# Kernel optimization log

Hardware: AMD Instinct MI355X
Metric: run time of the kernel (lower is better)

Reference implementation:

```python
import jax, jax.numpy as jnp
import numpy as np

H = 1024
NH = 16
HD = H // NH
EPS = 1e-5


def setup_inputs() -> dict:
    key = jax.random.key(0)
    ks = jax.random.split(key, 12)
    B, S = 4, 2048
    scale = 1.0 / np.sqrt(H)
    inp = {
        "x": jax.random.normal(ks[0], (B, S, H), jnp.float32),
        "mask": jnp.ones((B, S), jnp.int32),
        "Wq": jax.random.normal(ks[1], (H, H), jnp.float32) * scale,
        "bq": jnp.zeros((H,), jnp.float32),
        "Wk": jax.random.normal(ks[2], (H, H), jnp.float32) * scale,
        "bk": jnp.zeros((H,), jnp.float32),
        "Wv": jax.random.normal(ks[3], (H, H), jnp.float32) * scale,
        "bv": jnp.zeros((H,), jnp.float32),
        "Wo": jax.random.normal(ks[4], (H, H), jnp.float32) * scale,
        "bo": jnp.zeros((H,), jnp.float32),
        "gamma": jnp.ones((H,), jnp.float32),
        "beta": jnp.zeros((H,), jnp.float32),
    }
    return inp


def reference(x, mask, Wq, bq, Wk, bk, Wv, bv, Wo, bo, gamma, beta):
    B, S, _ = x.shape
    # QKV projections -> [B, NH, S, HD]
    def split_heads(t):
        return t.reshape(B, S, NH, HD).transpose(0, 2, 1, 3)
    q = split_heads(x @ Wq.T + bq)
    k = split_heads(x @ Wk.T + bk)
    v = split_heads(x @ Wv.T + bv)
    # scaled dot-product scores [B, NH, S, S]
    scores = jnp.einsum("bhqd,bhkd->bhqk", q, k) / np.sqrt(HD).astype(np.float32)
    m = (mask[:, None, None, :] == 0)  # [B,1,1,S]
    scores = jnp.where(m, -1e9, scores)
    attn = jax.nn.softmax(scores, axis=-1)
    # dropout is identity at eval time
    attended = jnp.einsum("bhqk,bhkd->bhqd", attn, v)
    attended = attended.transpose(0, 2, 1, 3).reshape(B, S, H)
    out = attended @ Wo.T + bo
    # residual + LayerNorm
    y = x + out
    mu = jnp.mean(y, axis=-1, keepdims=True)
    var = jnp.mean(jnp.square(y - mu), axis=-1, keepdims=True)
    return (y - mu) * jax.lax.rsqrt(var + EPS) * gamma + beta
```

## Files before the change

### kernel.cpp

```cpp
#include <hip/hip_runtime.h>
#include <stdint.h>

#define HDIM 1024
#define NHEAD 16
#define HD 64
#define NB 4
#define SEQ 2048
#define NROWS (NB*SEQ)
#define NBH (NB*NHEAD)

typedef __attribute__((ext_vector_type(8))) short short8;
typedef __attribute__((ext_vector_type(4))) float f32x4;

typedef __attribute__((address_space(1))) const void gk_t;
typedef __attribute__((address_space(3))) void lds_t;

static __device__ __forceinline__ unsigned short f2bf(float f) {
  union { float f; unsigned u; } v; v.f = f;
  unsigned r = v.u + 0x7fffu + ((v.u >> 16) & 1u);
  return (unsigned short)(r >> 16);
}

__global__ __launch_bounds__(256) void cvt_f32_bf16(const float* __restrict__ in,
                                                    unsigned short* __restrict__ out,
                                                    int n4) {
  int i = blockIdx.x * 256 + threadIdx.x;
  if (i >= n4) return;
  float4 v = reinterpret_cast<const float4*>(in)[i];
  ushort4 o;
  o.x = f2bf(v.x); o.y = f2bf(v.y); o.z = f2bf(v.z); o.w = f2bf(v.w);
  reinterpret_cast<ushort4*>(out)[i] = o;
}

__global__ __launch_bounds__(256) void cvt_weights(
    const float* __restrict__ Wq, const float* __restrict__ Wk,
    const float* __restrict__ Wv, const float* __restrict__ Wo,
    unsigned short* __restrict__ wqkv, unsigned short* __restrict__ wo) {
  int which = blockIdx.x >> 10;
  int i = (blockIdx.x & 1023) * 256 + threadIdx.x;
  const float* src = (which == 0) ? Wq : (which == 1) ? Wk : (which == 2) ? Wv : Wo;
  unsigned short* dst = (which < 3) ? (wqkv + (size_t)which * 1048576) : wo;
  float4 v = reinterpret_cast<const float4*>(src)[i];
  ushort4 o;
  o.x = f2bf(v.x); o.y = f2bf(v.y); o.z = f2bf(v.z); o.w = f2bf(v.w);
  reinterpret_cast<ushort4*>(dst)[i] = o;
}

__global__ __launch_bounds__(256) void mask_prep(const int* __restrict__ mask,
                                                 float* __restrict__ fb,
                                                 unsigned* __restrict__ flags) {
  if (blockIdx.x < 32) {
    int i = blockIdx.x * 256 + threadIdx.x;
    fb[i] = (mask[i] == 0) ? -1e9f : 0.0f;
  } else {
    int i = threadIdx.x;
    __shared__ unsigned char sh[128];
    if (i < 128) {
      int b = i >> 5, t = i & 31;
      const int* mrow = mask + b * SEQ + t * 64;
      int any = 0;
#pragma unroll 8
      for (int j = 0; j < 64; ++j) any |= (mrow[j] == 0);
      sh[i] = (unsigned char)any;
    }
    __syncthreads();
    if (i < NB) {
      unsigned f = 0;
      for (int t2 = 0; t2 < 32; ++t2) f |= (sh[i * 32 + t2] ? 1u : 0u) << t2;
      flags[i] = f;
    }
  }
}

static __device__ __forceinline__ void gemm_mainloop(
    const unsigned short* __restrict__ A, const unsigned short* __restrict__ B,
    int rowA0, int rowB0,
    unsigned short* As, unsigned short* Bs,
    f32x4 acc[4][4]) {
  const int tid  = threadIdx.x;
  const int lane = tid & 63;
  const int wave = tid >> 6;
  const int wm = wave >> 1, wn = wave & 1;
  const int srow = lane >> 3;
  const int scol = (lane & 7) << 3;

  for (int kt = 0; kt < 1024; kt += 64) {
    __syncthreads();
#pragma unroll
    for (int i = 0; i < 4; ++i) {
      int c = wave * 4 + i;
      const unsigned short* ga = A + (size_t)(rowA0 + c * 8 + srow) * 1024 + kt + scol;
      const unsigned short* gb = B + (size_t)(rowB0 + c * 8 + srow) * 1024 + kt + scol;
      __builtin_amdgcn_global_load_lds((gk_t*)ga, (lds_t*)(As + c * 512), 16, 0, 0);
      __builtin_amdgcn_global_load_lds((gk_t*)gb, (lds_t*)(Bs + c * 512), 16, 0, 0);
    }
    __syncthreads();
#pragma unroll
    for (int kk = 0; kk < 2; ++kk) {
      short8 af[4], bfr[4];
#pragma unroll
      for (int mi = 0; mi < 4; ++mi)
        af[mi] = *reinterpret_cast<const short8*>(
            As + (wm * 64 + mi * 16 + (lane & 15)) * 64 + kk * 32 + ((lane >> 4) << 3));
#pragma unroll
      for (int ni = 0; ni < 4; ++ni)
        bfr[ni] = *reinterpret_cast<const short8*>(
            Bs + (wn * 64 + ni * 16 + (lane & 15)) * 64 + kk * 32 + ((lane >> 4) << 3));
#pragma unroll
      for (int mi = 0; mi < 4; ++mi)
#pragma unroll
        for (int ni = 0; ni < 4; ++ni)
          acc[mi][ni] = __builtin_amdgcn_mfma_f32_16x16x32_bf16(af[mi], bfr[ni], acc[mi][ni], 0, 0, 0);
    }
  }
}

__global__ __launch_bounds__(256) void gemm_qkv(
    const unsigned short* __restrict__ xb, const unsigned short* __restrict__ wqkv,
    const float* __restrict__ bq, const float* __restrict__ bk, const float* __restrict__ bv,
    unsigned short* __restrict__ qout, unsigned short* __restrict__ kout,
    unsigned short* __restrict__ vtout) {
  __shared__ __align__(16) unsigned short As[128 * 64];
  __shared__ __align__(16) unsigned short Bs[128 * 64];
  f32x4 acc[4][4];
  const f32x4 zero = {0.f, 0.f, 0.f, 0.f};
#pragma unroll
  for (int i = 0; i < 4; ++i)
#pragma unroll
    for (int j = 0; j < 4; ++j) acc[i][j] = zero;

  int flat = blockIdx.y * 24 + blockIdx.x;
  int s = (flat & 7) * 192 + (flat >> 3);
  int by = s / 24, bx = s - by * 24;
  const int bm0 = by * 128;
  const int bn0 = bx * 128;
  gemm_mainloop(xb, wqkv, bm0, bn0, As, Bs, acc);

  const int lane = threadIdx.x & 63, wave = threadIdx.x >> 6;
  const int wm = wave >> 1, wn = wave & 1;
#pragma unroll
  for (int mi = 0; mi < 4; ++mi) {
    int m0 = bm0 + wm * 64 + mi * 16 + ((lane >> 4) << 2);
#pragma unroll
    for (int ni = 0; ni < 4; ++ni) {
      int n = bn0 + wn * 64 + ni * 16 + (lane & 15);
      int which = n >> 10;
      int nc = n & 1023;
      float bias = (which == 0 ? bq : which == 1 ? bk : bv)[nc];
      int h = nc >> 6, d = nc & 63;
#pragma unroll
      for (int r = 0; r < 4; ++r) {
        int m = m0 + r;
        int b = m >> 11, ss = m & 2047;
        float v = acc[mi][ni][r] + bias;
        if (which == 0) v *= 0.18033688011112042f;
        unsigned short val = f2bf(v);
        int bh = b * NHEAD + h;
        if (which == 2) {
          vtout[(((size_t)bh * HD + d) << 11) + ss] = val;
        } else {
          unsigned short* dst = (which == 0) ? qout : kout;
          dst[(((size_t)bh << 11) + ss) * HD + d] = val;
        }
      }
    }
  }
}

__global__ __launch_bounds__(256) void gemm_proj(
    const unsigned short* __restrict__ ab, const unsigned short* __restrict__ wob,
    const float* __restrict__ bo, const float* __restrict__ x, float* __restrict__ y) {
  __shared__ __align__(16) unsigned short As[128 * 64];
  __shared__ __align__(16) unsigned short Bs[128 * 64];
  f32x4 acc[4][4];
  const f32x4 zero = {0.f, 0.f, 0.f, 0.f};
#pragma unroll
  for (int i = 0; i < 4; ++i)
#pragma unroll
    for (int j = 0; j < 4; ++j) acc[i][j] = zero;

  int flat = blockIdx.y * 8 + blockIdx.x;
  int s = (flat & 7) * 64 + (flat >> 3);
  int by = s >> 3, bx = s & 7;
  const int bm0 = by * 128;
  const int bn0 = bx * 128;
  gemm_mainloop(ab, wob, bm0, bn0, As, Bs, acc);

  const int lane = threadIdx.x & 63, wave = threadIdx.x >> 6;
  const int wm = wave >> 1, wn = wave & 1;
#pragma unroll
  for (int mi = 0; mi < 4; ++mi) {
    int m0 = bm0 + wm * 64 + mi * 16 + ((lane >> 4) << 2);
#pragma unroll
    for (int ni = 0; ni < 4; ++ni) {
      int n = bn0 + wn * 64 + ni * 16 + (lane & 15);
      float bias = bo[n];
#pragma unroll
      for (int r = 0; r < 4; ++r) {
        size_t idx = (size_t)(m0 + r) * HDIM + n;
        y[idx] = acc[mi][ni][r] + bias + x[idx];
      }
    }
  }
}

__global__ __launch_bounds__(512) void flash_attn(
    const unsigned short* __restrict__ Q, const unsigned short* __restrict__ K,
    const unsigned short* __restrict__ VT, const float* __restrict__ fbias,
    const unsigned* __restrict__ mflagsPtr,
    unsigned short* __restrict__ O) {
  __shared__ __align__(16) char Ks[2][64 * 128];
  __shared__ __align__(16) char Vs[2][64 * 128];
  __shared__ __align__(16) char Ps[8 * 16 * 128];

  const int tid = threadIdx.x;
  const int lane = tid & 63, wave = tid >> 6;
  const int l15 = lane & 15, g = lane >> 4;
  const int bh = blockIdx.y;
  const int b = bh >> 4, h = bh & 15;
  const int q0 = blockIdx.x * 128;

  const unsigned short* qptr = Q + ((size_t)bh * SEQ + q0 + wave * 16 + l15) * HD + g * 8;
  short8 qf0 = *reinterpret_cast<const short8*>(qptr);
  short8 qf1 = *reinterpret_cast<const short8*>(qptr + 32);

  const f32x4 zero = {0.f, 0.f, 0.f, 0.f};
  f32x4 oacc[4];
#pragma unroll
  for (int i = 0; i < 4; ++i) oacc[i] = zero;
  f32x4 lacc = zero;
  const unsigned mflags = mflagsPtr[b];

  short8 ones;
#pragma unroll
  for (int i = 0; i < 8; ++i) ones[i] = (short)0x3F80;

  const int srow = tid >> 3;
  const int scol = (tid & 7) << 3;
  const int swzs = (srow & 7) << 4;
  const int stoff = srow * 128 + ((scol * 2) ^ swzs);
  char* kd0 = Ks[0] + stoff; char* kd1 = Ks[1] + stoff;
  char* vd0 = Vs[0] + stoff; char* vd1 = Vs[1] + stoff;
  const unsigned short* kg = K + ((size_t)bh * SEQ + srow) * HD + scol;
  const unsigned short* vg = VT + (((size_t)bh * HD + srow) << 11) + scol;

  const int cfrag = g << 4;
  const int swzr = (l15 & 7) << 4;
  const float* fbrow = fbias + b * SEQ;
  char* prow = Ps + wave * 2048 + l15 * 128;

  short8 kp = *reinterpret_cast<const short8*>(kg);
  short8 vp = *reinterpret_cast<const short8*>(vg);
  *reinterpret_cast<short8*>(kd0) = kp;
  *reinterpret_cast<short8*>(vd0) = vp;
  kp = *reinterpret_cast<const short8*>(kg + (size_t)64 * HD);
  vp = *reinterpret_cast<const short8*>(vg + 64);
  __syncthreads();

  auto step = [&](int jt, const char* Kr, const char* Vr, char* Kw, char* Vw) {
    f32x4 sf[4];
    __builtin_amdgcn_s_setprio(1);
#pragma unroll
    for (int ni = 0; ni < 4; ++ni) {
      const char* kr = Kr + (ni * 16 + l15) * 128;
      short8 a0 = *reinterpret_cast<const short8*>(kr + (cfrag ^ swzr));
      short8 a1 = *reinterpret_cast<const short8*>(kr + ((cfrag + 64) ^ swzr));
      f32x4 t = __builtin_amdgcn_mfma_f32_16x16x32_bf16(a0, qf0, zero, 0, 0, 0);
      sf[ni] = __builtin_amdgcn_mfma_f32_16x16x32_bf16(a1, qf1, t, 0, 0, 0);
    }
    __builtin_amdgcn_s_setprio(0);

    if (jt + 1 < SEQ / 64) {
      *reinterpret_cast<short8*>(Kw) = kp;
      *reinterpret_cast<short8*>(Vw) = vp;
    }

    if (__builtin_amdgcn_readfirstlane((mflags >> jt) & 1u)) {
#pragma unroll
      for (int ni = 0; ni < 4; ++ni) {
        f32x4 fbv = *reinterpret_cast<const f32x4*>(fbrow + jt * 64 + ni * 16 + 4 * g);
#pragma unroll
        for (int r = 0; r < 4; ++r) sf[ni][r] += fbv[r];
      }
    }

#pragma unroll
    for (int ni = 0; ni < 4; ++ni)
#pragma unroll
      for (int r = 0; r < 4; ++r)
        sf[ni][r] = __builtin_amdgcn_exp2f(sf[ni][r]);

#pragma unroll
    for (int ni = 0; ni < 4; ++ni) {
      unsigned lo_, hi_;
      asm("v_cvt_pk_bf16_f32 %0, %1, %2" : "=v"(lo_) : "v"(sf[ni][0]), "v"(sf[ni][1]));
      asm("v_cvt_pk_bf16_f32 %0, %1, %2" : "=v"(hi_) : "v"(sf[ni][2]), "v"(sf[ni][3]));
      *reinterpret_cast<uint2*>(prow + ((32 * ni + 8 * g) ^ swzr)) = make_uint2(lo_, hi_);
    }
    asm volatile("s_waitcnt lgkmcnt(0)" ::: "memory");
    __builtin_amdgcn_sched_barrier(0);
    short8 pb0 = *reinterpret_cast<const short8*>(prow + (cfrag ^ swzr));
    short8 pb1 = *reinterpret_cast<const short8*>(prow + ((cfrag + 64) ^ swzr));

    __builtin_amdgcn_s_setprio(1);
#pragma unroll
    for (int di = 0; di < 4; ++di) {
      const char* vr = Vr + (di * 16 + l15) * 128;
      short8 va0 = *reinterpret_cast<const short8*>(vr + (cfrag ^ swzr));
      short8 va1 = *reinterpret_cast<const short8*>(vr + ((cfrag + 64) ^ swzr));
      oacc[di] = __builtin_amdgcn_mfma_f32_16x16x32_bf16(va0, pb0, oacc[di], 0, 0, 0);
      oacc[di] = __builtin_amdgcn_mfma_f32_16x16x32_bf16(va1, pb1, oacc[di], 0, 0, 0);
    }
    lacc = __builtin_amdgcn_mfma_f32_16x16x32_bf16(ones, pb0, lacc, 0, 0, 0);
    lacc = __builtin_amdgcn_mfma_f32_16x16x32_bf16(ones, pb1, lacc, 0, 0, 0);
    __builtin_amdgcn_s_setprio(0);

    if (jt + 2 < SEQ / 64) {
      kp = *reinterpret_cast<const short8*>(kg + (size_t)(jt + 2) * 64 * HD);
      vp = *reinterpret_cast<const short8*>(vg + (jt + 2) * 64);
    }
  };

  for (int jt = 0; jt < SEQ / 64; jt += 2) {
    step(jt,     Ks[0], Vs[0], kd1, vd1);
    __syncthreads();
    step(jt + 1, Ks[1], Vs[1], kd0, vd0);
    __syncthreads();
  }

  {
    float inv = 1.0f / lacc[0];
    char* orow_lds = Ps + (wave * 16 + l15) * 128;
#pragma unroll
    for (int di = 0; di < 4; ++di) {
      float e0 = oacc[di][0] * inv, e1 = oacc[di][1] * inv;
      float e2 = oacc[di][2] * inv, e3 = oacc[di][3] * inv;
      unsigned lo_, hi_;
      asm("v_cvt_pk_bf16_f32 %0, %1, %2" : "=v"(lo_) : "v"(e0), "v"(e1));
      asm("v_cvt_pk_bf16_f32 %0, %1, %2" : "=v"(hi_) : "v"(e2), "v"(e3));
      char* dst = orow_lds + ((32 * di + 8 * g) ^ swzr);
      *reinterpret_cast<uint2*>(dst) = make_uint2(lo_, hi_);
    }
  }
  __syncthreads();
  {
    int q = tid >> 2;
    int c4 = tid & 3;
    int swz = (q & 7) << 4;
    const char* src = Ps + q * 128;
    short8 o0 = *reinterpret_cast<const short8*>(src + ((c4 * 32) ^ swz));
    short8 o1 = *reinterpret_cast<const short8*>(src + ((c4 * 32 + 16) ^ swz));
    unsigned short* orow = O + ((size_t)b * SEQ + q0 + q) * HDIM + h * 64 + c4 * 16;
    *reinterpret_cast<short8*>(orow) = o0;
    *reinterpret_cast<short8*>(orow + 8) = o1;
  }
}

__global__ __launch_bounds__(256) void layernorm(float* __restrict__ y,
                                                 const float* __restrict__ gamma,
                                                 const float* __restrict__ beta) {
  const int row = blockIdx.x;
  float* yr = y + (size_t)row * HDIM;
  const int tid = threadIdx.x;
  float4 v = reinterpret_cast<const float4*>(yr)[tid];
  float s = v.x + v.y + v.z + v.w;
  float s2 = v.x * v.x + v.y * v.y + v.z * v.z + v.w * v.w;
#pragma unroll
  for (int off = 1; off < 64; off <<= 1) {
    s += __shfl_xor(s, off);
    s2 += __shfl_xor(s2, off);
  }
  __shared__ float red[8];
  const int wave = tid >> 6, lane = tid & 63;
  if (lane == 0) { red[wave] = s; red[wave + 4] = s2; }
  __syncthreads();
  s = red[0] + red[1] + red[2] + red[3];
  s2 = red[4] + red[5] + red[6] + red[7];
  float mean = s * (1.f / HDIM);
  float var = s2 * (1.f / HDIM) - mean * mean;
  float rstd = rsqrtf(var + 1e-5f);
  float4 g = reinterpret_cast<const float4*>(gamma)[tid];
  float4 bt = reinterpret_cast<const float4*>(beta)[tid];
  float4 o;
  o.x = (v.x - mean) * rstd * g.x + bt.x;
  o.y = (v.y - mean) * rstd * g.y + bt.y;
  o.z = (v.z - mean) * rstd * g.z + bt.z;
  o.w = (v.w - mean) * rstd * g.w + bt.w;
  reinterpret_cast<float4*>(yr)[tid] = o;
}

extern "C" void kernel_launch(void* const* d_in, const int* in_sizes, int n_in,
                              void* d_out, int out_size, void* d_ws, size_t ws_size,
                              hipStream_t stream) {
  (void)in_sizes; (void)n_in; (void)out_size; (void)ws_size;
  const float* x     = (const float*)d_in[0];
  const int*   mask  = (const int*)d_in[1];
  const float* Wq    = (const float*)d_in[2];
  const float* bq    = (const float*)d_in[3];
  const float* Wk    = (const float*)d_in[4];
  const float* bk    = (const float*)d_in[5];
  const float* Wv    = (const float*)d_in[6];
  const float* bv    = (const float*)d_in[7];
  const float* Wo    = (const float*)d_in[8];
  const float* bo    = (const float*)d_in[9];
  const float* gamma = (const float*)d_in[10];
  const float* beta  = (const float*)d_in[11];
  float* out = (float*)d_out;

  char* ws = (char*)d_ws;
  unsigned short* xb   = (unsigned short*)(ws);
  unsigned short* wqkv = (unsigned short*)(ws + 16777216);
  unsigned short* wo   = (unsigned short*)(ws + 16777216 + 6291456);
  unsigned short* q    = (unsigned short*)(ws + 25165824);
  unsigned short* k    = (unsigned short*)(ws + 25165824 + 16777216);
  unsigned short* vt   = (unsigned short*)(ws + 25165824 + 2 * 16777216);
  unsigned short* attn = xb;
  float* fbias = (float*)(ws + 16777216);
  unsigned* mflags = (unsigned*)(ws + 16777216 + NB * SEQ * 4);

  cvt_f32_bf16<<<8192, 256, 0, stream>>>(x, xb, NROWS * HDIM / 4);
  cvt_weights<<<4096, 256, 0, stream>>>(Wq, Wk, Wv, Wo, wqkv, wo);

  gemm_qkv<<<dim3(24, 64), 256, 0, stream>>>(xb, wqkv, bq, bk, bv, q, k, vt);
  mask_prep<<<33, 256, 0, stream>>>(mask, fbias, mflags);
  flash_attn<<<dim3(16, 64), 512, 0, stream>>>(q, k, vt, fbias, mflags, attn);
  gemm_proj<<<dim3(8, 64), 256, 0, stream>>>(attn, wo, bo, x, out);
  layernorm<<<NROWS, 256, 0, stream>>>(out, gamma, beta);
}
```

Before: 247.2 us.

## Double-buffer GEMM mainloop with swizzled LDS and 256-row tiles

Replaces the GEMM mainloop with a 256x128 tile version run by 512 threads (8 waves). The next K-tile is prefetched into a second LDS buffer while MFMAs run on the current one, and rows are XOR-swizzled to avoid LDS bank conflicts. The MFMA block is wrapped in s_setprio. The intent is to hide global-load latency, halve the number of blocks, and cut one barrier per iteration. In exchange it uses 96KB of LDS per block, which limits occupancy, and the QKV GEMM grid drops to 768 blocks.

After: 232.3 us. 1.06x faster.

```diff
diff --git a/kernel.cpp b/kernel.cpp
--- a/kernel.cpp
+++ b/kernel.cpp
@@ -72,56 +72,89 @@
   }
 }
 
-static __device__ __forceinline__ void gemm_mainloop(
+static __device__ __forceinline__ void gemm_mainloop256(
     const unsigned short* __restrict__ A, const unsigned short* __restrict__ B,
     int rowA0, int rowB0,
-    unsigned short* As, unsigned short* Bs,
+    char* As , char* Bs ,
     f32x4 acc[4][4]) {
   const int tid  = threadIdx.x;
   const int lane = tid & 63;
   const int wave = tid >> 6;
+  const int l15 = lane & 15, g = lane >> 4;
   const int wm = wave >> 1, wn = wave & 1;
-  const int srow = lane >> 3;
-  const int scol = (lane & 7) << 3;
-
-  for (int kt = 0; kt < 1024; kt += 64) {
+  const int srow8 = lane >> 3;
+  const int schunk = lane & 7;
+
+  const int wbase = wave * 1024;
+
+#define STAGE_TILE(buf, kt)                                                        \
+  {                                                                                \
+    _Pragma("unroll")                                                              \
+    for (int a = 0; a < 4; ++a) {                                                  \
+      int row = a * 64 + wave * 8 + srow8;                                         \
+      int chunk = schunk ^ (row & 7);                                              \
+      const unsigned short* ga = A + (size_t)(rowA0 + row) * 1024 + (kt) + chunk * 8; \
+      __builtin_amdgcn_global_load_lds((gk_t*)ga,                                  \
+          (lds_t*)(As + (buf) * 32768 + a * 8192 + wbase), 16, 0, 0);              \
+    }                                                                              \
+    _Pragma("unroll")                                                              \
+    for (int a = 0; a < 2; ++a) {                                                  \
+      int row = a * 64 + wave * 8 + srow8;                                         \
+      int chunk = schunk ^ (row & 7);                                              \
+      const unsigned short* gb = B + (size_t)(rowB0 + row) * 1024 + (kt) + chunk * 8; \
+      __builtin_amdgcn_global_load_lds((gk_t*)gb,                                  \
+          (lds_t*)(Bs + (buf) * 16384 + a * 8192 + wbase), 16, 0, 0);              \
+    }                                                                              \
+  }
+
+  STAGE_TILE(0, 0);
+  __syncthreads();
+
+  for (int t = 0; t < 16; ++t) {
+    if (t + 1 < 16) STAGE_TILE((t + 1) & 1, (t + 1) * 64);
+
+    const char* Ab = As + (t & 1) * 32768;
+    const char* Bb = Bs + (t & 1) * 16384;
+    short8 af[2][4], bfr[2][4];
+#pragma unroll
+    for (int ks = 0; ks < 2; ++ks)
+#pragma unroll
+      for (int mi = 0; mi < 4; ++mi) {
+        int row = wm * 64 + mi * 16 + l15;
+        af[ks][mi] = *reinterpret_cast<const short8*>(
+            Ab + row * 128 + (((ks * 4 + g) ^ (row & 7)) << 4));
+      }
+#pragma unroll
+    for (int ks = 0; ks < 2; ++ks)
+#pragma unroll
+      for (int ni = 0; ni < 4; ++ni) {
+        int row = wn * 64 + ni * 16 + l15;
+        bfr[ks][ni] = *reinterpret_cast<const short8*>(
+            Bb + row * 128 + (((ks * 4 + g) ^ (row & 7)) << 4));
+      }
+
+    __builtin_amdgcn_s_setprio(1);
+#pragma unroll
+    for (int ks = 0; ks < 2; ++ks)
+#pragma unroll
+      for (int mi = 0; mi < 4; ++mi)
+#pragma unroll
+        for (int ni = 0; ni < 4; ++ni)
+          acc[mi][ni] = __builtin_amdgcn_mfma_f32_16x16x32_bf16(
+              af[ks][mi], bfr[ks][ni], acc[mi][ni], 0, 0, 0);
+    __builtin_amdgcn_s_setprio(0);
     __syncthreads();
-#pragma unroll
-    for (int i = 0; i < 4; ++i) {
-      int c = wave * 4 + i;
-      const unsigned short* ga = A + (size_t)(rowA0 + c * 8 + srow) * 1024 + kt + scol;
-      const unsigned short* gb = B + (size_t)(rowB0 + c * 8 + srow) * 1024 + kt + scol;
-      __builtin_amdgcn_global_load_lds((gk_t*)ga, (lds_t*)(As + c * 512), 16, 0, 0);
-      __builtin_amdgcn_global_load_lds((gk_t*)gb, (lds_t*)(Bs + c * 512), 16, 0, 0);
-    }
-    __syncthreads();
-#pragma unroll
-    for (int kk = 0; kk < 2; ++kk) {
-      short8 af[4], bfr[4];
-#pragma unroll
-      for (int mi = 0; mi < 4; ++mi)
-        af[mi] = *reinterpret_cast<const short8*>(
-            As + (wm * 64 + mi * 16 + (lane & 15)) * 64 + kk * 32 + ((lane >> 4) << 3));
-#pragma unroll
-      for (int ni = 0; ni < 4; ++ni)
-        bfr[ni] = *reinterpret_cast<const short8*>(
-            Bs + (wn * 64 + ni * 16 + (lane & 15)) * 64 + kk * 32 + ((lane >> 4) << 3));
-#pragma unroll
-      for (int mi = 0; mi < 4; ++mi)
-#pragma unroll
-        for (int ni = 0; ni < 4; ++ni)
-          acc[mi][ni] = __builtin_amdgcn_mfma_f32_16x16x32_bf16(af[mi], bfr[ni], acc[mi][ni], 0, 0, 0);
-    }
-  }
-}
-
-__global__ __launch_bounds__(256) void gemm_qkv(
+  }
+#undef STAGE_TILE
+}
+
+__global__ __launch_bounds__(512) void gemm_qkv(
     const unsigned short* __restrict__ xb, const unsigned short* __restrict__ wqkv,
     const float* __restrict__ bq, const float* __restrict__ bk, const float* __restrict__ bv,
     unsigned short* __restrict__ qout, unsigned short* __restrict__ kout,
     unsigned short* __restrict__ vtout) {
-  __shared__ __align__(16) unsigned short As[128 * 64];
-  __shared__ __align__(16) unsigned short Bs[128 * 64];
+  __shared__ __align__(16) char As[2 * 32768];
+  __shared__ __align__(16) char Bs[2 * 16384];
   f32x4 acc[4][4];
   const f32x4 zero = {0.f, 0.f, 0.f, 0.f};
 #pragma unroll
@@ -130,20 +163,21 @@
     for (int j = 0; j < 4; ++j) acc[i][j] = zero;
 
   int flat = blockIdx.y * 24 + blockIdx.x;
-  int s = (flat & 7) * 192 + (flat >> 3);
+  int s = (flat & 7) * 96 + (flat >> 3);
   int by = s / 24, bx = s - by * 24;
-  const int bm0 = by * 128;
+  const int bm0 = by * 256;
   const int bn0 = bx * 128;
-  gemm_mainloop(xb, wqkv, bm0, bn0, As, Bs, acc);
+  gemm_mainloop256(xb, wqkv, bm0, bn0, As, Bs, acc);
 
   const int lane = threadIdx.x & 63, wave = threadIdx.x >> 6;
+  const int l15 = lane & 15, g = lane >> 4;
   const int wm = wave >> 1, wn = wave & 1;
 #pragma unroll
   for (int mi = 0; mi < 4; ++mi) {
-    int m0 = bm0 + wm * 64 + mi * 16 + ((lane >> 4) << 2);
+    int m0 = bm0 + wm * 64 + mi * 16 + g * 4;
 #pragma unroll
     for (int ni = 0; ni < 4; ++ni) {
-      int n = bn0 + wn * 64 + ni * 16 + (lane & 15);
+      int n = bn0 + wn * 64 + ni * 16 + l15;
       int which = n >> 10;
       int nc = n & 1023;
       float bias = (which == 0 ? bq : which == 1 ? bk : bv)[nc];
@@ -167,11 +201,11 @@
   }
 }
 
-__global__ __launch_bounds__(256) void gemm_proj(
+__global__ __launch_bounds__(512) void gemm_proj(
     const unsigned short* __restrict__ ab, const unsigned short* __restrict__ wob,
     const float* __restrict__ bo, const float* __restrict__ x, float* __restrict__ y) {
-  __shared__ __align__(16) unsigned short As[128 * 64];
-  __shared__ __align__(16) unsigned short Bs[128 * 64];
+  __shared__ __align__(16) char As[2 * 32768];
+  __shared__ __align__(16) char Bs[2 * 16384];
   f32x4 acc[4][4];
   const f32x4 zero = {0.f, 0.f, 0.f, 0.f};
 #pragma unroll
@@ -180,20 +214,21 @@
     for (int j = 0; j < 4; ++j) acc[i][j] = zero;
 
   int flat = blockIdx.y * 8 + blockIdx.x;
-  int s = (flat & 7) * 64 + (flat >> 3);
+  int s = (flat & 7) * 32 + (flat >> 3);
   int by = s >> 3, bx = s & 7;
-  const int bm0 = by * 128;
+  const int bm0 = by * 256;
   const int bn0 = bx * 128;
-  gemm_mainloop(ab, wob, bm0, bn0, As, Bs, acc);
+  gemm_mainloop256(ab, wob, bm0, bn0, As, Bs, acc);
 
   const int lane = threadIdx.x & 63, wave = threadIdx.x >> 6;
+  const int l15 = lane & 15, g = lane >> 4;
   const int wm = wave >> 1, wn = wave & 1;
 #pragma unroll
   for (int mi = 0; mi < 4; ++mi) {
-    int m0 = bm0 + wm * 64 + mi * 16 + ((lane >> 4) << 2);
+    int m0 = bm0 + wm * 64 + mi * 16 + g * 4;
 #pragma unroll
     for (int ni = 0; ni < 4; ++ni) {
-      int n = bn0 + wn * 64 + ni * 16 + (lane & 15);
+      int n = bn0 + wn * 64 + ni * 16 + l15;
       float bias = bo[n];
 #pragma unroll
       for (int r = 0; r < 4; ++r) {
@@ -421,9 +456,9 @@
   cvt_f32_bf16<<<8192, 256, 0, stream>>>(x, xb, NROWS * HDIM / 4);
   cvt_weights<<<4096, 256, 0, stream>>>(Wq, Wk, Wv, Wo, wqkv, wo);
 
-  gemm_qkv<<<dim3(24, 64), 256, 0, stream>>>(xb, wqkv, bq, bk, bv, q, k, vt);
+  gemm_qkv<<<dim3(24, 32), 512, 0, stream>>>(xb, wqkv, bq, bk, bv, q, k, vt);
   mask_prep<<<33, 256, 0, stream>>>(mask, fbias, mflags);
   flash_attn<<<dim3(16, 64), 512, 0, stream>>>(q, k, vt, fbias, mflags, attn);
-  gemm_proj<<<dim3(8, 64), 256, 0, stream>>>(attn, wo, bo, x, out);
+  gemm_proj<<<dim3(8, 32), 512, 0, stream>>>(attn, wo, bo, x, out);
   layernorm<<<NROWS, 256, 0, stream>>>(out, gamma, beta);
 }
```
